# Performance work log

Hardware: AMD Instinct MI355X
Metric: run time of the kernel (lower is better)

## Reference

```python
import jax, jax.numpy as jnp
import numpy as np

DISP_RANGE = 10
OUT_D = 2 * DISP_RANGE + 1  # 21


def _shear_by_dim3(x):
    # x: [b, a, d, n3, n4]; for each index along dim3 (size m), roll along d by
    # shift = m//2 - index, zeroing wrapped-around entries (matches torch.roll + zero fill).
    b, a, d, m, n4 = x.shape
    shifts = m // 2 - jnp.arange(m)                      # [m]
    src = jnp.arange(d)[None, :] - shifts[:, None]       # [m, d]; out[j] = in[j - shift]
    valid = ((src >= 0) & (src < d)).astype(x.dtype)     # [m, d]
    src_c = jnp.clip(src, 0, d - 1)
    xt = jnp.transpose(x, (0, 1, 3, 4, 2))               # [b, a, m, n4, d]
    g = jnp.take_along_axis(xt, src_c[None, None, :, None, :], axis=4)
    g = g * valid[None, None, :, None, :]
    return jnp.transpose(g, (0, 1, 4, 2, 3))             # back to [b, a, d, m, n4]


def _pool_matrix(a, d):
    # Dense [a, OUT_D, d] matrix replicating, per angular index, the centered slice
    # d//2 - DISP_RANGE*a_delta : d//2 + DISP_RANGE*a_delta + 1 followed by
    # F.adaptive_avg_pool1d(., OUT_D): bin k averages [floor(k*L/OUT_D), ceil((k+1)*L/OUT_D)).
    P = np.zeros((a, OUT_D, d), dtype=np.float32)
    for i in range(a):
        a_delta = max(abs(i - a // 2), 1)
        L = 2 * DISP_RANGE * a_delta + 1
        start0 = d // 2 - DISP_RANGE * a_delta
        for k in range(OUT_D):
            s = (k * L) // OUT_D
            e = -((-(k + 1) * L) // OUT_D)  # ceil division
            P[i, k, start0 + s:start0 + e] = 1.0 / (e - s)
    return P


def setup_inputs() -> dict:
    key = jax.random.key(0)
    k1, k2 = jax.random.split(key)
    shp = (8, 9, 128, 64, 64)
    return {
        "attn_map_uh": jax.random.normal(k1, shp, dtype=jnp.float32),
        "attn_map_vw": jax.random.normal(k2, shp, dtype=jnp.float32),
    }


def reference(attn_map_uh, attn_map_vw):
    b, a, d, h, w = attn_map_uh.shape
    uh = _shear_by_dim3(attn_map_uh)                               # shear per h
    vw = _shear_by_dim3(jnp.swapaxes(attn_map_vw, -1, -2))         # shear per w
    vw = jnp.swapaxes(vw, -1, -2)
    attn_map = jnp.stack([uh, vw], axis=1)                         # [b, 2, a, d, h, w]
    d_eff = d
    if DISP_RANGE * (a // 2) * 2 + 1 > d:
        pad = (DISP_RANGE * (a // 2) * 2 - d) // 2 + 1
        attn_map = jnp.pad(attn_map, ((0, 0), (0, 0), (0, 0), (pad, pad), (0, 0), (0, 0)))
        d_eff = d + 2 * pad
    P = jnp.asarray(_pool_matrix(a, d_eff))                        # [a, 21, d_eff]
    # Variable-window adaptive average pooling as a single contraction over d.
    cost_volume = jnp.einsum('bnadhw,akd->bnakhw', attn_map, P)    # [b, 2, a, 21, h, w]
    return cost_volume
```

## Files before the change

kernel.cpp:

```cpp
#include <hip/hip_runtime.h>

#define DISP_RANGE 10
#define OUT_D 21
#define B_ 8
#define A_ 9
#define D_ 128
#define HW_ 4096


template<int AD, int WID>
__device__ __forceinline__ void compute_group(
    const float* __restrict__ uh_slice,
    const float* lds,
    float* __restrict__ out0,
    float* __restrict__ out1,
    int h, int w)
{
    constexpr int L      = 2 * DISP_RANGE * AD + 1;
    constexpr int START0 = (D_ / 2) - DISP_RANGE * AD;
    constexpr int LO     = (START0 - 32 < 0) ? 0 : (START0 - 32);
    constexpr int HI     = (START0 + L + 31 > D_) ? D_ : (START0 + L + 31);
    constexpr int K0     = (WID == 0) ? 0 : (6 + 5 * (WID - 1));
    constexpr int K1     = K0 + ((WID == 0) ? 6 : 5);
    constexpr int NK     = K1 - K0;
    constexpr int S0     = (K0 * L) / OUT_D;
    constexpr int E1     = (K1 * L + OUT_D - 1) / OUT_D;

    float acc0[NK];
    float acc1[NK];
#pragma unroll
    for (int i = 0; i < NK; ++i) { acc0[i] = 0.0f; acc1[i] = 0.0f; }

#pragma unroll
    for (int dd = START0 + S0; dd < START0 + E1; ++dd) {
        const int  row  = dd - 32 + h;
        const bool ok0  = (row >= 0) && (row < D_);
        const int  rowc = row < 0 ? 0 : (row > D_ - 1 ? D_ - 1 : row);
        float v0 = uh_slice[(size_t)rowc * HW_ + (size_t)w];
        v0 = ok0 ? v0 : 0.0f;

        const int  rv   = dd - 32 + w;
        const bool ok1  = (rv >= LO) && (rv < HI);
        const int  rvc  = rv < LO ? LO : (rv > HI - 1 ? HI - 1 : rv);
        float v1 = lds[(rvc - LO) * 64 + w];
        v1 = ok1 ? v1 : 0.0f;

#pragma unroll
        for (int k = K0; k < K1; ++k) {
            if (dd >= START0 + (k * L) / OUT_D &&
                dd <  START0 + ((k + 1) * L + OUT_D - 1) / OUT_D) {
                acc0[k - K0] += v0;
                acc1[k - K0] += v1;
            }
        }
    }

#pragma unroll
    for (int k = K0; k < K1; ++k) {
        const int   s  = (k * L) / OUT_D;
        const int   e  = ((k + 1) * L + OUT_D - 1) / OUT_D;
        const float wt = 1.0f / (float)(e - s);
        out0[(size_t)k * HW_] = acc0[k - K0] * wt;
        out1[(size_t)k * HW_] = acc1[k - K0] * wt;
    }
}

template<int AD>
__device__ __forceinline__ void run_block(
    const float* __restrict__ uh,
    const float* __restrict__ vw,
    float* __restrict__ out,
    float* lds,
    int b, int a, int h, int t)
{
    constexpr int L      = 2 * DISP_RANGE * AD + 1;
    constexpr int START0 = (D_ / 2) - DISP_RANGE * AD;
    constexpr int LO     = (START0 - 32 < 0) ? 0 : (START0 - 32);
    constexpr int HI     = (START0 + L + 31 > D_) ? D_ : (START0 + L + 31);
    constexpr int NROWS  = HI - LO;
    constexpr int NCH    = NROWS / 4;

    const int lane = t & 63;
    const int w    = lane;
    const int wid  = t >> 6;

    const size_t plane = (size_t)(b * A_ + a) * D_ * HW_;
    const float* uh_slice = uh + plane + (size_t)h * 64;
    const float* vw_slice = vw + plane + (size_t)h * 64;

#pragma unroll
    for (int c = 0; c < NCH; ++c) {
        if ((c & 3) == wid) {
            const float* src = vw_slice
                + (size_t)(LO + c * 4 + (lane >> 4)) * HW_
                + (size_t)((lane & 15) * 4);
            __builtin_amdgcn_global_load_lds(
                (const __attribute__((address_space(1))) void*)src,
                (__attribute__((address_space(3))) void*)&lds[c * 256],
                16, 0, 0);
        }
    }
    __syncthreads();

    const size_t out_b0 = ((size_t)(b * 2) * A_ + a) * OUT_D * HW_
                        + (size_t)h * 64 + (size_t)w;
    const size_t out_b1 = out_b0 + (size_t)A_ * OUT_D * HW_;
    float* out0 = out + out_b0;
    float* out1 = out + out_b1;

    switch (wid) {
        case 0: compute_group<AD, 0>(uh_slice, lds, out0, out1, h, w); break;
        case 1: compute_group<AD, 1>(uh_slice, lds, out0, out1, h, w); break;
        case 2: compute_group<AD, 2>(uh_slice, lds, out0, out1, h, w); break;
        default: compute_group<AD, 3>(uh_slice, lds, out0, out1, h, w); break;
    }
}

__global__ __launch_bounds__(256) void cost_volume_kernel(
    const float* __restrict__ uh,
    const float* __restrict__ vw,
    float* __restrict__ out)
{
    __shared__ float lds[D_ * 64];

    const int h = blockIdx.x;
    const int a = blockIdx.y;
    const int b = blockIdx.z;
    const int t = (int)threadIdx.x;

    switch (a) {
        case 3: case 4: case 5:
            run_block<1>(uh, vw, out, lds, b, a, h, t); break;
        case 2: case 6:
            run_block<2>(uh, vw, out, lds, b, a, h, t); break;
        case 1: case 7:
            run_block<3>(uh, vw, out, lds, b, a, h, t); break;
        default:
            run_block<4>(uh, vw, out, lds, b, a, h, t); break;
    }
}

extern "C" void kernel_launch(void* const* d_in, const int* in_sizes, int n_in,
                              void* d_out, int out_size, void* d_ws, size_t ws_size,
                              hipStream_t stream) {
    const float* uh = (const float*)d_in[0];
    const float* vw = (const float*)d_in[1];
    float* out = (float*)d_out;

    dim3 grid(64, A_, B_);
    dim3 block(256);
    cost_volume_kernel<<<grid, block, 0, stream>>>(uh, vw, out);
}
```

Before: 42.01 us.

## Split uh and vw work into separate wave groups to overlap LDS fill with compute

Doubles the block to 512 threads. Waves 0-3 compute the uh half directly from global memory while waves 4-7 issue the asynchronous global-to-LDS loads for vw. The vw waves then wait at the barrier and compute the vw half from LDS. This is meant to hide the LDS fill latency behind the uh computation and to raise parallelism, at the cost of larger blocks and a launch-bounds change that may limit register use.

```diff
diff --git a/kernel.cpp b/kernel.cpp
--- a/kernel.cpp
+++ b/kernel.cpp
@@ -9,12 +9,52 @@
 
 
 template<int AD, int WID>
-__device__ __forceinline__ void compute_group(
+__device__ __forceinline__ void compute_uh(
     const float* __restrict__ uh_slice,
+    float* __restrict__ out0,
+    int h, int w)
+{
+    constexpr int L      = 2 * DISP_RANGE * AD + 1;
+    constexpr int START0 = (D_ / 2) - DISP_RANGE * AD;
+    constexpr int K0     = (WID == 0) ? 0 : (6 + 5 * (WID - 1));
+    constexpr int K1     = K0 + ((WID == 0) ? 6 : 5);
+    constexpr int NK     = K1 - K0;
+    constexpr int S0     = (K0 * L) / OUT_D;
+    constexpr int E1     = (K1 * L + OUT_D - 1) / OUT_D;
+
+    float acc[NK];
+#pragma unroll
+    for (int i = 0; i < NK; ++i) acc[i] = 0.0f;
+
+#pragma unroll
+    for (int dd = START0 + S0; dd < START0 + E1; ++dd) {
+        const int  row  = dd - 32 + h;
+        const bool ok   = (row >= 0) && (row < D_);
+        const int  rowc = row < 0 ? 0 : (row > D_ - 1 ? D_ - 1 : row);
+        float v = uh_slice[(size_t)rowc * HW_ + (size_t)w];
+        v = ok ? v : 0.0f;
+#pragma unroll
+        for (int k = K0; k < K1; ++k) {
+            if (dd >= START0 + (k * L) / OUT_D &&
+                dd <  START0 + ((k + 1) * L + OUT_D - 1) / OUT_D)
+                acc[k - K0] += v;
+        }
+    }
+
+#pragma unroll
+    for (int k = K0; k < K1; ++k) {
+        const int   s  = (k * L) / OUT_D;
+        const int   e  = ((k + 1) * L + OUT_D - 1) / OUT_D;
+        const float wt = 1.0f / (float)(e - s);
+        out0[(size_t)k * HW_] = acc[k - K0] * wt;
+    }
+}
+
+template<int AD, int WID>
+__device__ __forceinline__ void compute_vw(
     const float* lds,
-    float* __restrict__ out0,
     float* __restrict__ out1,
-    int h, int w)
+    int w)
 {
     constexpr int L      = 2 * DISP_RANGE * AD + 1;
     constexpr int START0 = (D_ / 2) - DISP_RANGE * AD;
@@ -26,32 +66,22 @@
     constexpr int S0     = (K0 * L) / OUT_D;
     constexpr int E1     = (K1 * L + OUT_D - 1) / OUT_D;
 
-    float acc0[NK];
-    float acc1[NK];
+    float acc[NK];
 #pragma unroll
-    for (int i = 0; i < NK; ++i) { acc0[i] = 0.0f; acc1[i] = 0.0f; }
+    for (int i = 0; i < NK; ++i) acc[i] = 0.0f;
 
 #pragma unroll
     for (int dd = START0 + S0; dd < START0 + E1; ++dd) {
-        const int  row  = dd - 32 + h;
-        const bool ok0  = (row >= 0) && (row < D_);
-        const int  rowc = row < 0 ? 0 : (row > D_ - 1 ? D_ - 1 : row);
-        float v0 = uh_slice[(size_t)rowc * HW_ + (size_t)w];
-        v0 = ok0 ? v0 : 0.0f;
-
-        const int  rv   = dd - 32 + w;
-        const bool ok1  = (rv >= LO) && (rv < HI);
-        const int  rvc  = rv < LO ? LO : (rv > HI - 1 ? HI - 1 : rv);
-        float v1 = lds[(rvc - LO) * 64 + w];
-        v1 = ok1 ? v1 : 0.0f;
-
+        const int  rv  = dd - 32 + w;
+        const bool ok  = (rv >= LO) && (rv < HI);
+        const int  rvc = rv < LO ? LO : (rv > HI - 1 ? HI - 1 : rv);
+        float v = lds[(rvc - LO) * 64 + w];
+        v = ok ? v : 0.0f;
 #pragma unroll
         for (int k = K0; k < K1; ++k) {
             if (dd >= START0 + (k * L) / OUT_D &&
-                dd <  START0 + ((k + 1) * L + OUT_D - 1) / OUT_D) {
-                acc0[k - K0] += v0;
-                acc1[k - K0] += v1;
-            }
+                dd <  START0 + ((k + 1) * L + OUT_D - 1) / OUT_D)
+                acc[k - K0] += v;
         }
     }
 
@@ -60,8 +90,7 @@
         const int   s  = (k * L) / OUT_D;
         const int   e  = ((k + 1) * L + OUT_D - 1) / OUT_D;
         const float wt = 1.0f / (float)(e - s);
-        out0[(size_t)k * HW_] = acc0[k - K0] * wt;
-        out1[(size_t)k * HW_] = acc1[k - K0] * wt;
+        out1[(size_t)k * HW_] = acc[k - K0] * wt;
     }
 }
 
@@ -88,35 +117,50 @@
     const float* uh_slice = uh + plane + (size_t)h * 64;
     const float* vw_slice = vw + plane + (size_t)h * 64;
 
+    if (wid >= 4) {
+        const int sg = wid - 4;
 #pragma unroll
-    for (int c = 0; c < NCH; ++c) {
-        if ((c & 3) == wid) {
-            const float* src = vw_slice
-                + (size_t)(LO + c * 4 + (lane >> 4)) * HW_
-                + (size_t)((lane & 15) * 4);
-            __builtin_amdgcn_global_load_lds(
-                (const __attribute__((address_space(1))) void*)src,
-                (__attribute__((address_space(3))) void*)&lds[c * 256],
-                16, 0, 0);
+        for (int c = 0; c < NCH; ++c) {
+            if ((c & 3) == sg) {
+                const float* src = vw_slice
+                    + (size_t)(LO + c * 4 + (lane >> 4)) * HW_
+                    + (size_t)((lane & 15) * 4);
+                __builtin_amdgcn_global_load_lds(
+                    (const __attribute__((address_space(1))) void*)src,
+                    (__attribute__((address_space(3))) void*)&lds[c * 256],
+                    16, 0, 0);
+            }
         }
     }
-    __syncthreads();
 
     const size_t out_b0 = ((size_t)(b * 2) * A_ + a) * OUT_D * HW_
                         + (size_t)h * 64 + (size_t)w;
     const size_t out_b1 = out_b0 + (size_t)A_ * OUT_D * HW_;
-    float* out0 = out + out_b0;
-    float* out1 = out + out_b1;
 
-    switch (wid) {
-        case 0: compute_group<AD, 0>(uh_slice, lds, out0, out1, h, w); break;
-        case 1: compute_group<AD, 1>(uh_slice, lds, out0, out1, h, w); break;
-        case 2: compute_group<AD, 2>(uh_slice, lds, out0, out1, h, w); break;
-        default: compute_group<AD, 3>(uh_slice, lds, out0, out1, h, w); break;
+    if (wid < 4) {
+        float* out0 = out + out_b0;
+        switch (wid) {
+            case 0: compute_uh<AD, 0>(uh_slice, out0, h, w); break;
+            case 1: compute_uh<AD, 1>(uh_slice, out0, h, w); break;
+            case 2: compute_uh<AD, 2>(uh_slice, out0, h, w); break;
+            default: compute_uh<AD, 3>(uh_slice, out0, h, w); break;
+        }
+    }
+
+    __syncthreads();
+
+    if (wid >= 4) {
+        float* out1 = out + out_b1;
+        switch (wid - 4) {
+            case 0: compute_vw<AD, 0>(lds, out1, w); break;
+            case 1: compute_vw<AD, 1>(lds, out1, w); break;
+            case 2: compute_vw<AD, 2>(lds, out1, w); break;
+            default: compute_vw<AD, 3>(lds, out1, w); break;
+        }
     }
 }
 
-__global__ __launch_bounds__(256) void cost_volume_kernel(
+__global__ __launch_bounds__(512, 8) void cost_volume_kernel(
     const float* __restrict__ uh,
     const float* __restrict__ vw,
     float* __restrict__ out)
@@ -148,6 +192,6 @@
     float* out = (float*)d_out;
 
     dim3 grid(64, A_, B_);
-    dim3 block(256);
+    dim3 block(512);
     cost_volume_kernel<<<grid, block, 0, stream>>>(uh, vw, out);
 }
```

After: 42.83 us. About the same (+1.9%).

## Double-buffer vw LDS staging across four batches per block with 8 waves

Applied to the files above, without the earlier changes.

Each block now processes four batch indices in sequence. The vw tile for the next batch is loaded into registers and written to a second LDS buffer while the current batch is computed, replacing the single direct global-to-LDS load per block. The block grows to 512 threads and the 21 output bins are split across 8 waves instead of 4. This is meant to hide load latency and amortize block setup. In exchange the block uses twice the LDS, the grid is four times smaller, and the staging goes through registers.

```diff
diff --git a/kernel.cpp b/kernel.cpp
--- a/kernel.cpp
+++ b/kernel.cpp
@@ -6,137 +6,183 @@
 #define A_ 9
 #define D_ 128
 #define HW_ 4096
+#define NT 4
 
 
+template<int AD> struct G {
+    static constexpr int L      = 2 * DISP_RANGE * AD + 1;
+    static constexpr int START0 = 64 - DISP_RANGE * AD;
+    static constexpr int LO     = (START0 - 32 < 0) ? 0 : (START0 - 32);
+    static constexpr int HI     = (START0 + L + 31 > D_) ? D_ : (START0 + L + 31);
+    static constexpr int NROWS  = HI - LO;
+    static constexpr int NCH    = NROWS / 4;
+};
+
+template<int WID> struct KG {
+    static constexpr int K0 = (WID < 5) ? 3 * WID : 15 + 2 * (WID - 5);
+    static constexpr int NK = (WID < 5) ? 3 : 2;
+    static constexpr int K1 = K0 + NK;
+};
+
+template<int AD, int WID> struct ST {
+    static constexpr int K = (G<AD>::NCH - WID + 7) / 8;
+};
+
 template<int AD, int WID>
-__device__ __forceinline__ void compute_group(
+__device__ __forceinline__ void stage_load(const float* __restrict__ vw_slice,
+                                           float4* r, int lane) {
+#pragma unroll
+    for (int j = 0; j < ST<AD, WID>::K; ++j) {
+        const int c = WID + 8 * j;
+        r[j] = *reinterpret_cast<const float4*>(
+            vw_slice + (size_t)(G<AD>::LO + c * 4 + (lane >> 4)) * HW_
+                     + (size_t)((lane & 15) * 4));
+    }
+}
+
+template<int AD, int WID>
+__device__ __forceinline__ void stage_write(float* buf, const float4* r, int lane) {
+#pragma unroll
+    for (int j = 0; j < ST<AD, WID>::K; ++j) {
+        const int c = WID + 8 * j;
+        *reinterpret_cast<float4*>(&buf[c * 256 + (lane >> 4) * 64 + (lane & 15) * 4]) = r[j];
+    }
+}
+
+template<int AD, int WID>
+__device__ __forceinline__ void compute_tile(
     const float* __restrict__ uh_slice,
-    const float* lds,
+    const float* buf,
     float* __restrict__ out0,
     float* __restrict__ out1,
     int h, int w)
 {
-    constexpr int L      = 2 * DISP_RANGE * AD + 1;
-    constexpr int START0 = (D_ / 2) - DISP_RANGE * AD;
-    constexpr int LO     = (START0 - 32 < 0) ? 0 : (START0 - 32);
-    constexpr int HI     = (START0 + L + 31 > D_) ? D_ : (START0 + L + 31);
-    constexpr int K0     = (WID == 0) ? 0 : (6 + 5 * (WID - 1));
-    constexpr int K1     = K0 + ((WID == 0) ? 6 : 5);
-    constexpr int NK     = K1 - K0;
-    constexpr int S0     = (K0 * L) / OUT_D;
-    constexpr int E1     = (K1 * L + OUT_D - 1) / OUT_D;
+    using g = G<AD>; using kg = KG<WID>;
+    constexpr int S0 = (kg::K0 * g::L) / OUT_D;
+    constexpr int E1 = (kg::K1 * g::L + OUT_D - 1) / OUT_D;
 
-    float acc0[NK];
-    float acc1[NK];
+    float acc0[kg::NK];
+    float acc1[kg::NK];
 #pragma unroll
-    for (int i = 0; i < NK; ++i) { acc0[i] = 0.0f; acc1[i] = 0.0f; }
+    for (int i = 0; i < kg::NK; ++i) { acc0[i] = 0.0f; acc1[i] = 0.0f; }
 
 #pragma unroll
-    for (int dd = START0 + S0; dd < START0 + E1; ++dd) {
+    for (int dd = g::START0 + S0; dd < g::START0 + E1; ++dd) {
         const int  row  = dd - 32 + h;
         const bool ok0  = (row >= 0) && (row < D_);
         const int  rowc = row < 0 ? 0 : (row > D_ - 1 ? D_ - 1 : row);
         float v0 = uh_slice[(size_t)rowc * HW_ + (size_t)w];
         v0 = ok0 ? v0 : 0.0f;
 
-        const int  rv   = dd - 32 + w;
-        const bool ok1  = (rv >= LO) && (rv < HI);
-        const int  rvc  = rv < LO ? LO : (rv > HI - 1 ? HI - 1 : rv);
-        float v1 = lds[(rvc - LO) * 64 + w];
+        const int  rv  = dd - 32 + w;
+        const bool ok1 = (rv >= g::LO) && (rv < g::HI);
+        const int  rvc = rv < g::LO ? g::LO : (rv > g::HI - 1 ? g::HI - 1 : rv);
+        float v1 = buf[(rvc - g::LO) * 64 + w];
         v1 = ok1 ? v1 : 0.0f;
 
 #pragma unroll
-        for (int k = K0; k < K1; ++k) {
-            if (dd >= START0 + (k * L) / OUT_D &&
-                dd <  START0 + ((k + 1) * L + OUT_D - 1) / OUT_D) {
-                acc0[k - K0] += v0;
-                acc1[k - K0] += v1;
+        for (int k = kg::K0; k < kg::K1; ++k) {
+            if (dd >= g::START0 + (k * g::L) / OUT_D &&
+                dd <  g::START0 + ((k + 1) * g::L + OUT_D - 1) / OUT_D) {
+                acc0[k - kg::K0] += v0;
+                acc1[k - kg::K0] += v1;
             }
         }
     }
 
 #pragma unroll
-    for (int k = K0; k < K1; ++k) {
-        const int   s  = (k * L) / OUT_D;
-        const int   e  = ((k + 1) * L + OUT_D - 1) / OUT_D;
+    for (int k = kg::K0; k < kg::K1; ++k) {
+        const int   s  = (k * g::L) / OUT_D;
+        const int   e  = ((k + 1) * g::L + OUT_D - 1) / OUT_D;
         const float wt = 1.0f / (float)(e - s);
-        out0[(size_t)k * HW_] = acc0[k - K0] * wt;
-        out1[(size_t)k * HW_] = acc1[k - K0] * wt;
+        out0[(size_t)k * HW_] = acc0[k - kg::K0] * wt;
+        out1[(size_t)k * HW_] = acc1[k - kg::K0] * wt;
     }
 }
 
+template<int AD, int WID>
+__device__ __forceinline__ void run_pipe(
+    const float* __restrict__ uh, const float* __restrict__ vw,
+    float* __restrict__ out, float* buf0, float* buf1,
+    int b0, int a, int h, int lane)
+{
+    float4 r[ST<AD, WID>::K];
+
+    const size_t pl0      = (size_t)(b0 * A_ + a) * D_ * HW_ + (size_t)h * 64;
+    const size_t pstride  = (size_t)A_ * D_ * HW_;
+    const size_t ob0      = ((size_t)(b0 * 2) * A_ + a) * OUT_D * HW_
+                          + (size_t)h * 64 + (size_t)lane;
+    const size_t obstride = (size_t)2 * A_ * OUT_D * HW_;
+    const size_t o01      = (size_t)A_ * OUT_D * HW_;
+
+    stage_load<AD, WID>(vw + pl0, r, lane);
+    stage_write<AD, WID>(buf0, r, lane);
+
+    __syncthreads();
+    stage_load<AD, WID>(vw + pl0 + pstride, r, lane);
+    compute_tile<AD, WID>(uh + pl0, buf0,
+                          out + ob0, out + ob0 + o01, h, lane);
+    stage_write<AD, WID>(buf1, r, lane);
+
+    __syncthreads();
+    stage_load<AD, WID>(vw + pl0 + 2 * pstride, r, lane);
+    compute_tile<AD, WID>(uh + pl0 + pstride, buf1,
+                          out + ob0 + obstride, out + ob0 + obstride + o01, h, lane);
+    stage_write<AD, WID>(buf0, r, lane);
+
+    __syncthreads();
+    stage_load<AD, WID>(vw + pl0 + 3 * pstride, r, lane);
+    compute_tile<AD, WID>(uh + pl0 + 2 * pstride, buf0,
+                          out + ob0 + 2 * obstride, out + ob0 + 2 * obstride + o01, h, lane);
+    stage_write<AD, WID>(buf1, r, lane);
+
+    __syncthreads();
+    compute_tile<AD, WID>(uh + pl0 + 3 * pstride, buf1,
+                          out + ob0 + 3 * obstride, out + ob0 + 3 * obstride + o01, h, lane);
+}
+
 template<int AD>
-__device__ __forceinline__ void run_block(
-    const float* __restrict__ uh,
-    const float* __restrict__ vw,
-    float* __restrict__ out,
-    float* lds,
-    int b, int a, int h, int t)
+__device__ __forceinline__ void run_ad(
+    const float* __restrict__ uh, const float* __restrict__ vw,
+    float* __restrict__ out, float* buf0, float* buf1,
+    int b0, int a, int h, int lane, int wid)
 {
-    constexpr int L      = 2 * DISP_RANGE * AD + 1;
-    constexpr int START0 = (D_ / 2) - DISP_RANGE * AD;
-    constexpr int LO     = (START0 - 32 < 0) ? 0 : (START0 - 32);
-    constexpr int HI     = (START0 + L + 31 > D_) ? D_ : (START0 + L + 31);
-    constexpr int NROWS  = HI - LO;
-    constexpr int NCH    = NROWS / 4;
-
-    const int lane = t & 63;
-    const int w    = lane;
-    const int wid  = t >> 6;
-
-    const size_t plane = (size_t)(b * A_ + a) * D_ * HW_;
-    const float* uh_slice = uh + plane + (size_t)h * 64;
-    const float* vw_slice = vw + plane + (size_t)h * 64;
-
-#pragma unroll
-    for (int c = 0; c < NCH; ++c) {
-        if ((c & 3) == wid) {
-            const float* src = vw_slice
-                + (size_t)(LO + c * 4 + (lane >> 4)) * HW_
-                + (size_t)((lane & 15) * 4);
-            __builtin_amdgcn_global_load_lds(
-                (const __attribute__((address_space(1))) void*)src,
-                (__attribute__((address_space(3))) void*)&lds[c * 256],
-                16, 0, 0);
-        }
-    }
-    __syncthreads();
-
-    const size_t out_b0 = ((size_t)(b * 2) * A_ + a) * OUT_D * HW_
-                        + (size_t)h * 64 + (size_t)w;
-    const size_t out_b1 = out_b0 + (size_t)A_ * OUT_D * HW_;
-    float* out0 = out + out_b0;
-    float* out1 = out + out_b1;
-
     switch (wid) {
-        case 0: compute_group<AD, 0>(uh_slice, lds, out0, out1, h, w); break;
-        case 1: compute_group<AD, 1>(uh_slice, lds, out0, out1, h, w); break;
-        case 2: compute_group<AD, 2>(uh_slice, lds, out0, out1, h, w); break;
-        default: compute_group<AD, 3>(uh_slice, lds, out0, out1, h, w); break;
+        case 0: run_pipe<AD, 0>(uh, vw, out, buf0, buf1, b0, a, h, lane); break;
+        case 1: run_pipe<AD, 1>(uh, vw, out, buf0, buf1, b0, a, h, lane); break;
+        case 2: run_pipe<AD, 2>(uh, vw, out, buf0, buf1, b0, a, h, lane); break;
+        case 3: run_pipe<AD, 3>(uh, vw, out, buf0, buf1, b0, a, h, lane); break;
+        case 4: run_pipe<AD, 4>(uh, vw, out, buf0, buf1, b0, a, h, lane); break;
+        case 5: run_pipe<AD, 5>(uh, vw, out, buf0, buf1, b0, a, h, lane); break;
+        case 6: run_pipe<AD, 6>(uh, vw, out, buf0, buf1, b0, a, h, lane); break;
+        default: run_pipe<AD, 7>(uh, vw, out, buf0, buf1, b0, a, h, lane); break;
     }
 }
 
-__global__ __launch_bounds__(256) void cost_volume_kernel(
+__global__ __launch_bounds__(512, 4) void cost_volume_kernel(
     const float* __restrict__ uh,
     const float* __restrict__ vw,
     float* __restrict__ out)
 {
-    __shared__ float lds[D_ * 64];
+    __shared__ float buf0[D_ * 64];
+    __shared__ float buf1[D_ * 64];
 
-    const int h = blockIdx.x;
-    const int a = blockIdx.y;
-    const int b = blockIdx.z;
-    const int t = (int)threadIdx.x;
+    const int h  = blockIdx.x;
+    const int a  = blockIdx.y;
+    const int b0 = (int)blockIdx.z * NT;
+    const int t  = (int)threadIdx.x;
+    const int lane = t & 63;
+    const int wid  = t >> 6;
 
     switch (a) {
         case 3: case 4: case 5:
-            run_block<1>(uh, vw, out, lds, b, a, h, t); break;
+            run_ad<1>(uh, vw, out, buf0, buf1, b0, a, h, lane, wid); break;
         case 2: case 6:
-            run_block<2>(uh, vw, out, lds, b, a, h, t); break;
+            run_ad<2>(uh, vw, out, buf0, buf1, b0, a, h, lane, wid); break;
         case 1: case 7:
-            run_block<3>(uh, vw, out, lds, b, a, h, t); break;
+            run_ad<3>(uh, vw, out, buf0, buf1, b0, a, h, lane, wid); break;
         default:
-            run_block<4>(uh, vw, out, lds, b, a, h, t); break;
+            run_ad<4>(uh, vw, out, buf0, buf1, b0, a, h, lane, wid); break;
     }
 }
 
@@ -147,7 +193,7 @@
     const float* vw = (const float*)d_in[1];
     float* out = (float*)d_out;
 
-    dim3 grid(64, A_, B_);
-    dim3 block(256);
+    dim3 grid(64, A_, B_ / NT);
+    dim3 block(512);
     cost_volume_kernel<<<grid, block, 0, stream>>>(uh, vw, out);
 }
```

Measured after the change: 46.19 us. 10.0% more time.
